# Performance work log

Measured on AMD Instinct MI355X. Metric: run time of the kernel, lower is better.

The kernel has to match this reference:

```python
import jax, jax.numpy as jnp
import numpy as np

B, S_LONG, S_SHORT, C_IN, H, D_STATE = 16384, 100, 10, 4, 64, 16
BN_EPS = 1e-5


def setup_inputs() -> dict:
    key = jax.random.key(0)
    ks = jax.random.split(key, 32)
    n = lambda i, shape, s=0.1: (jax.random.normal(ks[i], shape, dtype=jnp.float32) * s)
    inp = {
        "x": jax.random.normal(ks[0], (B, S_LONG, C_IN), dtype=jnp.float32),
        # ConvolutionalEyes (Conv1d weights are [out, in, k])
        "conv1_w": n(1, (H, C_IN, 3)), "conv1_b": n(2, (H,)),
        "conv2_w": n(3, (H, H, 5)),    "conv2_b": n(4, (H,)),
        "conv3_w": n(5, (H, H, 7)),    "conv3_b": n(6, (H,)),
        # BatchNorm1d (eval mode: running_mean=0, running_var=1)
        "bn1_g": jnp.ones((H,)), "bn1_b": jnp.zeros((H,)),
        "bn2_g": jnp.ones((H,)), "bn2_b": jnp.zeros((H,)),
        "bn3_g": jnp.ones((H,)), "bn3_b": jnp.zeros((H,)),
        # input_proj
        "proj_w": n(7, (C_IN, H)), "proj_b": n(8, (H,)),
        # MambaBlock (proj_in exists in torch code but is unused in forward)
        "A": n(9, (D_STATE, D_STATE)),
        "Bm": n(10, (H, D_STATE)),
        "Cm": n(11, (D_STATE, H)),
        "out_w": n(12, (H, H)), "out_b": n(13, (H,)),
        # ContextualGate
        "g1_w": n(14, (2 * H, H)), "g1_b": n(15, (H,)),
        "g2_w": n(16, (H, H)),     "g2_b": n(17, (H,)),
        # trading head
        "h1_w": n(18, (H, 32)), "h1_b": n(19, (32,)),
        "h2_w": n(20, (32, 3)), "h2_b": n(21, (3,)),
    }
    return inp


def _conv_bn_relu(x, w, b, g, beta, pad):
    # x: [B, C, L], w: [O, I, K]
    y = jax.lax.conv_general_dilated(x, w, (1,), [(pad, pad)],
                                     dimension_numbers=("NCW", "OIW", "NCW"))
    y = y + b[None, :, None]
    # eval-mode BN with running_mean=0, running_var=1
    y = g[None, :, None] * y * jax.lax.rsqrt(jnp.float32(1.0 + BN_EPS)) + beta[None, :, None]
    return jax.nn.relu(y)


def reference(x, conv1_w, conv1_b, conv2_w, conv2_b, conv3_w, conv3_b,
              bn1_g, bn1_b, bn2_g, bn2_b, bn3_g, bn3_b,
              proj_w, proj_b, A, Bm, Cm, out_w, out_b,
              g1_w, g1_b, g2_w, g2_b, h1_w, h1_b, h2_w, h2_b):
    # --- split windows ---
    x_short = x[:, -S_SHORT:, :]          # [B, 10, 4]
    x_long = x                            # [B, 100, 4]

    # --- ConvolutionalEyes (dropout = identity in eval) ---
    xc = jnp.swapaxes(x_short, 1, 2)      # [B, 4, 10]
    xc = _conv_bn_relu(xc, conv1_w, conv1_b, bn1_g, bn1_b, 1)
    xc = _conv_bn_relu(xc, conv2_w, conv2_b, bn2_g, bn2_b, 2)
    xc = _conv_bn_relu(xc, conv3_w, conv3_b, bn3_g, bn3_b, 3)
    short_features = jnp.mean(xc, axis=2)  # [B, 64]

    # --- input projection ---
    xp = x_long @ proj_w + proj_b          # [B, 100, 64]

    # --- MambaBlock: sequential scan over time ---
    def step(h, x_t):                      # h: [B, 16], x_t: [B, 64]
        h = jnp.tanh(x_t @ Bm + h @ A.T)
        return h, h @ Cm                   # y_t: [B, 64]

    h0 = jnp.zeros((x.shape[0], D_STATE), dtype=x.dtype)
    _, ys = jax.lax.scan(step, h0, jnp.swapaxes(xp, 0, 1))  # ys: [100, B, 64]
    long_context = ys[-1] @ out_w + out_b  # proj_out applied, last timestep

    # --- ContextualGate ---
    combined = jnp.concatenate([short_features, long_context], axis=1)  # [B, 128]
    gate = jax.nn.sigmoid(jnp.tanh(combined @ g1_w + g1_b) @ g2_w + g2_b)
    filtered = short_features * gate

    # --- trading head (dropout = identity in eval) ---
    logits = jax.nn.relu(filtered @ h1_w + h1_b) @ h2_w + h2_b  # [B, 3]
    return logits
```

## Files before the change

kernel.cpp:

```cpp
#include <hip/hip_runtime.h>
#include <cstddef>

#define NB 16384
#define TS 720
#define NRNN (NB/64)

typedef __attribute__((ext_vector_type(8))) _Float16 half8;
typedef __attribute__((ext_vector_type(4))) _Float16 half4;
typedef __attribute__((ext_vector_type(4))) float f32x4;
typedef __attribute__((ext_vector_type(2))) float f32x2;
typedef __attribute__((ext_vector_type(16))) float f32x16;

#define OFF_W1T 0
#define OFF_SC1 768
#define OFF_SH1 832
#define OFF_SC2 896
#define OFF_SH2 960
#define OFF_SC3 1024
#define OFF_SH3 1088
#define OFF_PB  1152
#define OFF_PBB 1216
#define OFF_W2H 2304
#define OFF_W2L 12544
#define OFF_W3H 22784
#define OFF_W3L 37120
#define OFF_SF  51456
#define OFF_H   (51456 + NB*64)
#define OFF_TF  1362176

#define G1H 0
#define G1L 8192
#define G2H 16384
#define G2L 20480
#define H1H 24576
#define H1L 26624
#define H2H 28672
#define H2L 29184
#define COH 29696
#define COL 30720
#define TFH 31744

static __device__ __forceinline__ f32x16 mfma32(half8 a, half8 b, f32x16 c) {
  return __builtin_amdgcn_mfma_f32_32x32x16_f16(a, b, c, 0, 0, 0);
}
static __device__ __forceinline__ f32x4 mfma16(half4 a, half4 b, f32x4 c) {
  return __builtin_amdgcn_mfma_f32_16x16x16f16(a, b, c, 0, 0, 0);
}
static __device__ __forceinline__ f32x4 mfma16k32(half8 a, half8 b, f32x4 c) {
  return __builtin_amdgcn_mfma_f32_16x16x32_f16(a, b, c, 0, 0, 0);
}

__global__ __launch_bounds__(256) void prep_kernel(
    const float* __restrict__ conv1_w, const float* __restrict__ conv1_b,
    const float* __restrict__ conv2_w, const float* __restrict__ conv2_b,
    const float* __restrict__ conv3_w, const float* __restrict__ conv3_b,
    const float* __restrict__ bn1_g, const float* __restrict__ bn1_b,
    const float* __restrict__ bn2_g, const float* __restrict__ bn2_b,
    const float* __restrict__ bn3_g, const float* __restrict__ bn3_b,
    const float* __restrict__ proj_w, const float* __restrict__ proj_b,
    const float* __restrict__ A, const float* __restrict__ Bm,
    const float* __restrict__ Cm, const float* __restrict__ out_w,
    const float* __restrict__ g1_w, const float* __restrict__ g2_w,
    const float* __restrict__ h1_w, const float* __restrict__ h2_w,
    float* __restrict__ ws)
{
  int tid = blockIdx.x * blockDim.x + threadIdx.x;
  int nt = gridDim.x * blockDim.x;
  const float s = rsqrtf(1.0f + 1e-5f);

  for (int i = tid; i < 64*12; i += nt) {
    int o = i & 63, rk = i >> 6;
    ws[OFF_W1T + i] = conv1_w[o*12 + rk];
  }
  for (int o = tid; o < 64; o += nt) {
    float s1 = bn1_g[o]*s, s2 = bn2_g[o]*s, s3 = bn3_g[o]*s;
    ws[OFF_SC1+o] = s1; ws[OFF_SH1+o] = s1*conv1_b[o] + bn1_b[o];
    ws[OFF_SC2+o] = s2; ws[OFF_SH2+o] = s2*conv2_b[o] + bn2_b[o];
    ws[OFF_SC3+o] = s3; ws[OFF_SH3+o] = s3*conv3_b[o] + bn3_b[o];
  }
  {
    _Float16* w2h = (_Float16*)(ws + OFF_W2H);
    _Float16* w2l = (_Float16*)(ws + OFF_W2L);
    for (int i = tid; i < 20*2*64; i += nt) {
      int lane = i & 63, ot = (i >> 6) & 1, sk = i >> 7;
      int tap = sk >> 2, ic0 = (sk & 3)*16 + (lane >> 5)*8;
      int o = ot*32 + (lane & 31);
      #pragma unroll
      for (int j = 0; j < 8; ++j) {
        float w = conv2_w[o*320 + (ic0 + j)*5 + tap];
        _Float16 hi = (_Float16)w;
        w2h[(size_t)i*8 + j] = hi;
        w2l[(size_t)i*8 + j] = (_Float16)(w - (float)hi);
      }
    }
  }
  {
    _Float16* w3h = (_Float16*)(ws + OFF_W3H);
    _Float16* w3l = (_Float16*)(ws + OFF_W3L);
    for (int i = tid; i < 28*2*64; i += nt) {
      int lane = i & 63, ot = (i >> 6) & 1, sk = i >> 7;
      int tap = sk >> 2, ic0 = (sk & 3)*16 + (lane >> 5)*8;
      int o = ot*32 + (lane & 31);
      #pragma unroll
      for (int j = 0; j < 8; ++j) {
        float w = conv3_w[o*448 + (ic0 + j)*7 + tap];
        _Float16 hi = (_Float16)w;
        w3h[(size_t)i*8 + j] = hi;
        w3l[(size_t)i*8 + j] = (_Float16)(w - (float)hi);
      }
    }
  }
  for (int i = tid; i < 64; i += nt) {
    int c = i >> 4, j = i & 15;
    float acc = 0.f;
    for (int m = 0; m < 64; ++m) acc += proj_w[c*64+m]*Bm[m*16+j];
    ws[OFF_PB + i] = acc;
  }
  for (int j = tid; j < 16; j += nt) {
    float acc = 0.f;
    for (int m = 0; m < 64; ++m) acc += proj_b[m]*Bm[m*16+j];
    ws[OFF_PBB + j] = acc;
  }

  _Float16* tf = (_Float16*)(ws + OFF_TF);
  for (int i = tid; i < 16*64; i += nt) {
    int l = i & 63, f = i >> 6, mt = f >> 2, ks = f & 3;
    int o = mt*16 + (l & 15), kb = ks*32 + (l >> 4)*8;
    #pragma unroll
    for (int j = 0; j < 8; ++j) {
      float w = g1_w[(size_t)(kb + j)*64 + o];
      _Float16 hi = (_Float16)w;
      tf[G1H + (size_t)i*8 + j] = hi;
      tf[G1L + (size_t)i*8 + j] = (_Float16)(w - (float)hi);
    }
  }
  for (int i = tid; i < 8*64; i += nt) {
    int l = i & 63, f = i >> 6, mt = f >> 1, ks = f & 1;
    int o = mt*16 + (l & 15), kb = ks*32 + (l >> 4)*8;
    #pragma unroll
    for (int j = 0; j < 8; ++j) {
      float w = g2_w[(size_t)(kb + j)*64 + o];
      _Float16 hi = (_Float16)w;
      tf[G2H + (size_t)i*8 + j] = hi;
      tf[G2L + (size_t)i*8 + j] = (_Float16)(w - (float)hi);
    }
  }
  for (int i = tid; i < 4*64; i += nt) {
    int l = i & 63, f = i >> 6, mt = f >> 1, ks = f & 1;
    int hx = mt*16 + (l & 15), kb = ks*32 + (l >> 4)*8;
    #pragma unroll
    for (int j = 0; j < 8; ++j) {
      float w = h1_w[(size_t)(kb + j)*32 + hx];
      _Float16 hi = (_Float16)w;
      tf[H1H + (size_t)i*8 + j] = hi;
      tf[H1L + (size_t)i*8 + j] = (_Float16)(w - (float)hi);
    }
  }
  for (int i = tid; i < 64; i += nt) {
    int l = i, m = l & 15, kb = (l >> 4)*8;
    #pragma unroll
    for (int j = 0; j < 8; ++j) {
      float w = (m < 3) ? h2_w[(size_t)(kb + j)*3 + m] : 0.f;
      _Float16 hi = (_Float16)w;
      tf[H2H + (size_t)i*8 + j] = hi;
      tf[H2L + (size_t)i*8 + j] = (_Float16)(w - (float)hi);
    }
  }
  for (int i = tid; i < 4*64; i += nt) {
    int l = i & 63, mt = i >> 6;
    int o = mt*16 + (l & 15), kb = (l >> 4)*4;
    #pragma unroll
    for (int j = 0; j < 4; ++j) {
      float acc = 0.f;
      for (int m = 0; m < 64; ++m) acc += Cm[(kb + j)*64 + m]*out_w[m*64 + o];
      _Float16 hi = (_Float16)acc;
      tf[COH + (size_t)i*4 + j] = hi;
      tf[COL + (size_t)i*4 + j] = (_Float16)(acc - (float)hi);
    }
  }
}

__global__ __launch_bounds__(256, 3) void conv123_kernel(
    const float* __restrict__ x, const float* __restrict__ wsr,
    const float* __restrict__ A, float* __restrict__ hout,
    float* __restrict__ sfp)
{
  __shared__ __align__(16) _Float16 ah[16][TS], al[16][TS];

  const int tid = threadIdx.x;
  const int lane = tid & 63;
  const int wid = tid >> 6;

  if (blockIdx.x < NRNN) {
    const int colb = lane & 15;
    const int q = lane >> 4;
    const size_t b = ((size_t)blockIdx.x*4 + wid)*16 + colb;

    const f32x4 av = *(const f32x4*)(A + (size_t)(lane & 15)*16 + q*4);
    half4 Ahi, Alo;
    #pragma unroll
    for (int j = 0; j < 4; ++j) {
      _Float16 hi = (_Float16)av[j];
      Ahi[j] = hi;
      Alo[j] = (_Float16)(av[j] - (float)hi);
    }
    f32x4 pb0 = *(const f32x4*)(wsr + OFF_PB + 0*16 + q*4);
    f32x4 pb1 = *(const f32x4*)(wsr + OFF_PB + 1*16 + q*4);
    f32x4 pb2 = *(const f32x4*)(wsr + OFF_PB + 2*16 + q*4);
    f32x4 pb3 = *(const f32x4*)(wsr + OFF_PB + 3*16 + q*4);
    f32x4 pbb = *(const f32x4*)(wsr + OFF_PBB + q*4);

    const float* xb = x + b*400;
    half4 hh = {}, hl = {};
    f32x4 hf;
    #pragma unroll 2
    for (int t = 0; t < 100; ++t) {
      const f32x4 xv = *(const f32x4*)(xb + t*4);
      f32x4 U;
      #pragma unroll
      for (int r = 0; r < 4; ++r)
        U[r] = pbb[r] + xv[0]*pb0[r] + xv[1]*pb1[r] + xv[2]*pb2[r] + xv[3]*pb3[r];
      f32x4 u = mfma16(Alo, hh, U);
      u = mfma16(Ahi, hl, u);
      u = mfma16(Ahi, hh, u);
      #pragma unroll
      for (int r = 0; r < 4; ++r) {
        float e = __expf(2.f*u[r]);
        float hn = 1.f - 2.f/(e + 1.f);
        hf[r] = hn;
        _Float16 hi = (_Float16)hn;
        hh[r] = hi;
        hl[r] = (_Float16)(hn - (float)hi);
      }
    }
    *(f32x4*)(hout + b*16 + q*4) = hf;
    return;
  }

  const int n = lane & 15;
  const int nc = (n < 10) ? n : 9;
  const int kh8 = (lane >> 5) * 8;
  const int rq = 4 * (lane >> 5);
  const int lbA = 4*wid + ((lane >> 4) & 1);
  const int lbB = lbA + 2;
  const half8 z8 = {};
  const size_t B0g = (size_t)(blockIdx.x - NRNN) * 16;

  {
    const float sc1 = wsr[OFF_SC1 + lane], sh1 = wsr[OFF_SH1 + lane];
    #pragma unroll
    for (int bb = 0; bb < 4; ++bb) {
      const int lb = 4*wid + bb;
      const size_t gb = B0g + lb;
      float xv[4][12];
      #pragma unroll
      for (int c = 0; c < 4; ++c) { xv[c][0] = 0.f; xv[c][11] = 0.f; }
      #pragma unroll
      for (int tt = 0; tt < 10; ++tt) {
        const f32x4 xt = *(const f32x4*)(x + gb*400 + (90 + tt)*4);
        #pragma unroll
        for (int c = 0; c < 4; ++c) xv[c][1 + tt] = xt[c];
      }
      float a1[10];
      #pragma unroll
      for (int t = 0; t < 10; ++t) a1[t] = 0.f;
      #pragma unroll
      for (int c = 0; c < 4; ++c)
        #pragma unroll
        for (int k = 0; k < 3; ++k) {
          const float wv = wsr[OFF_W1T + (c*3 + k)*64 + lane];
          #pragma unroll
          for (int t = 0; t < 10; ++t) a1[t] += wv * xv[c][t + k];
        }
      #pragma unroll
      for (int t = 0; t < 10; ++t) {
        float v = sc1*a1[t] + sh1;
        v = v > 0.f ? v : 0.f;
        _Float16 hi = (_Float16)v;
        ah[lb][t*72 + lane] = hi;
        al[lb][t*72 + lane] = (_Float16)(v - (float)hi);
      }
    }
  }

  const _Float16* bhpA = &ah[lbA][0];
  const _Float16* blpA = &al[lbA][0];
  const _Float16* bhpB = &ah[lbB][0];
  const _Float16* blpB = &al[lbB][0];
  const _Float16* w2h = (const _Float16*)(wsr + OFF_W2H);
  const _Float16* w2l = (const _Float16*)(wsr + OFF_W2L);
  const _Float16* w3h = (const _Float16*)(wsr + OFF_W3H);
  const _Float16* w3l = (const _Float16*)(wsr + OFF_W3L);
  const int lw8 = lane*8;

  {
    f32x16 a0A, a1A, a0B, a1B;
    #pragma unroll
    for (int r = 0; r < 16; ++r) { a0A[r] = 0.f; a1A[r] = 0.f; a0B[r] = 0.f; a1B[r] = 0.f; }
    #pragma unroll
    for (int sk = 0; sk < 20; ++sk) {
      const int tap = sk >> 2, icb = (sk & 3)*16;
      const int t = nc + tap - 2;
      const int tc = t < 0 ? 0 : (t > 9 ? 9 : t);
      const bool valid = (t >= 0) & (t <= 9);
      const int off = tc*72 + icb + kh8;
      half8 bhA = *(const half8*)(bhpA + off);
      half8 blA = *(const half8*)(blpA + off);
      half8 bhB = *(const half8*)(bhpB + off);
      half8 blB = *(const half8*)(blpB + off);
      bhA = valid ? bhA : z8;
      blA = valid ? blA : z8;
      bhB = valid ? bhB : z8;
      blB = valid ? blB : z8;
      const half8 wh0 = *(const half8*)(w2h + (size_t)(sk*2 + 0)*512 + lw8);
      const half8 wh1 = *(const half8*)(w2h + (size_t)(sk*2 + 1)*512 + lw8);
      const half8 wl0 = *(const half8*)(w2l + (size_t)(sk*2 + 0)*512 + lw8);
      const half8 wl1 = *(const half8*)(w2l + (size_t)(sk*2 + 1)*512 + lw8);
      a0A = mfma32(wh0, bhA, a0A);
      a0A = mfma32(wh0, blA, a0A);
      a0A = mfma32(wl0, bhA, a0A);
      a1A = mfma32(wh1, bhA, a1A);
      a1A = mfma32(wh1, blA, a1A);
      a1A = mfma32(wl1, bhA, a1A);
      a0B = mfma32(wh0, bhB, a0B);
      a0B = mfma32(wh0, blB, a0B);
      a0B = mfma32(wl0, bhB, a0B);
      a1B = mfma32(wh1, bhB, a1B);
      a1B = mfma32(wh1, blB, a1B);
      a1B = mfma32(wl1, bhB, a1B);
    }
    if (n < 10) {
      auto epi = [&](const f32x16& ac, int ot, int lb) {
        #pragma unroll
        for (int q = 0; q < 4; ++q) {
          const int rowb = 8*q + rq + ot*32;
          const f32x4 sc = *(const f32x4*)(wsr + OFF_SC2 + rowb);
          const f32x4 sh = *(const f32x4*)(wsr + OFF_SH2 + rowb);
          half4 h4, l4;
          #pragma unroll
          for (int r = 0; r < 4; ++r) {
            float v = sc[r]*ac[4*q + r] + sh[r];
            v = v > 0.f ? v : 0.f;
            _Float16 hi = (_Float16)v;
            h4[r] = hi;
            l4[r] = (_Float16)(v - (float)hi);
          }
          *(half4*)(&ah[lb][n*72 + rowb]) = h4;
          *(half4*)(&al[lb][n*72 + rowb]) = l4;
        }
      };
      epi(a0A, 0, lbA);
      epi(a1A, 1, lbA);
      epi(a0B, 0, lbB);
      epi(a1B, 1, lbB);
    }
  }

  {
    f32x16 b0A, b1A, b0B, b1B;
    #pragma unroll
    for (int r = 0; r < 16; ++r) { b0A[r] = 0.f; b1A[r] = 0.f; b0B[r] = 0.f; b1B[r] = 0.f; }
    #pragma unroll
    for (int sk = 0; sk < 28; ++sk) {
      const int tap = sk >> 2, icb = (sk & 3)*16;
      const int t = nc + tap - 3;
      const int tc = t < 0 ? 0 : (t > 9 ? 9 : t);
      const bool valid = (t >= 0) & (t <= 9);
      const int off = tc*72 + icb + kh8;
      half8 bhA = *(const half8*)(bhpA + off);
      half8 blA = *(const half8*)(blpA + off);
      half8 bhB = *(const half8*)(bhpB + off);
      half8 blB = *(const half8*)(blpB + off);
      bhA = valid ? bhA : z8;
      blA = valid ? blA : z8;
      bhB = valid ? bhB : z8;
      blB = valid ? blB : z8;
      const half8 wh0 = *(const half8*)(w3h + (size_t)(sk*2 + 0)*512 + lw8);
      const half8 wh1 = *(const half8*)(w3h + (size_t)(sk*2 + 1)*512 + lw8);
      const half8 wl0 = *(const half8*)(w3l + (size_t)(sk*2 + 0)*512 + lw8);
      const half8 wl1 = *(const half8*)(w3l + (size_t)(sk*2 + 1)*512 + lw8);
      b0A = mfma32(wh0, bhA, b0A);
      b0A = mfma32(wh0, blA, b0A);
      b0A = mfma32(wl0, bhA, b0A);
      b1A = mfma32(wh1, bhA, b1A);
      b1A = mfma32(wh1, blA, b1A);
      b1A = mfma32(wl1, bhA, b1A);
      b0B = mfma32(wh0, bhB, b0B);
      b0B = mfma32(wh0, blB, b0B);
      b0B = mfma32(wl0, bhB, b0B);
      b1B = mfma32(wh1, bhB, b1B);
      b1B = mfma32(wh1, blB, b1B);
      b1B = mfma32(wl1, bhB, b1B);
    }
    auto epi = [&](const f32x16& ac, int ot, int lb) {
      #pragma unroll
      for (int q = 0; q < 4; ++q) {
        const int rowb = 8*q + rq + ot*32;
        const f32x4 sc = *(const f32x4*)(wsr + OFF_SC3 + rowb);
        const f32x4 sh = *(const f32x4*)(wsr + OFF_SH3 + rowb);
        f32x4 v;
        #pragma unroll
        for (int r = 0; r < 4; ++r) {
          float t2 = sc[r]*ac[4*q + r] + sh[r];
          t2 = t2 > 0.f ? t2 : 0.f;
          v[r] = (n < 10) ? t2 : 0.f;
        }
        #pragma unroll
        for (int r = 0; r < 4; ++r) {
          v[r] += __shfl_xor(v[r], 1, 16);
          v[r] += __shfl_xor(v[r], 2, 16);
          v[r] += __shfl_xor(v[r], 4, 16);
          v[r] += __shfl_xor(v[r], 8, 16);
        }
        if (n == 0)
          *(f32x4*)(sfp + (B0g + lb)*64 + rowb) = v * 0.1f;
      }
    };
    epi(b0A, 0, lbA);
    epi(b1A, 1, lbA);
    epi(b0B, 0, lbB);
    epi(b1B, 1, lbB);
  }
}

#define CMBH 0
#define CMBL 2176
#define T1H  4352
#define T1L  5504
#define FLH  6656
#define FLL  7808
#define RH   8960
#define RL   9600
__global__ __launch_bounds__(256, 2) void tail_kernel(
    const float* __restrict__ wsr,
    const float* __restrict__ g1_b, const float* __restrict__ g2_b,
    const float* __restrict__ h1_b, const float* __restrict__ h2_b,
    const float* __restrict__ out_b, float* __restrict__ out)
{
  __shared__ __align__(16) _Float16 sAct[4*10240];

  const int tid = threadIdx.x;
  const int lane = tid & 63;
  const int wid = tid >> 6;
  const int n = lane & 15;
  const int q = lane >> 4;
  const int B0 = blockIdx.x*64 + wid*16;

  const _Float16* tfg = (const _Float16*)(wsr + OFF_TF);
  _Float16* wa = sAct + wid*10240;
  const float* sf = wsr + OFF_SF;
  const float* hws = wsr + OFF_H;

  const f32x4 hv = *(const f32x4*)(hws + (size_t)(B0 + n)*16 + q*4);
  half4 hh, hl;
  #pragma unroll
  for (int j = 0; j < 4; ++j) {
    _Float16 hi = (_Float16)hv[j];
    hh[j] = hi;
    hl[j] = (_Float16)(hv[j] - (float)hi);
  }
  f32x4 lc[4];
  #pragma unroll
  for (int mt = 0; mt < 4; ++mt) {
    lc[mt] = *(const f32x4*)(out_b + mt*16 + q*4);
    const half4 ah = *(const half4*)(tfg + COH + (size_t)(mt*64 + lane)*4);
    const half4 al = *(const half4*)(tfg + COL + (size_t)(mt*64 + lane)*4);
    lc[mt] = mfma16(al, hh, lc[mt]);
    lc[mt] = mfma16(ah, hl, lc[mt]);
    lc[mt] = mfma16(ah, hh, lc[mt]);
  }
  f32x4 sfv[4];
  #pragma unroll
  for (int mt = 0; mt < 4; ++mt) {
    sfv[mt] = *(const f32x4*)(sf + (size_t)(B0 + n)*64 + mt*16 + q*4);
    half4 sh4, sl4, lh4, ll4;
    #pragma unroll
    for (int r = 0; r < 4; ++r) {
      _Float16 hi = (_Float16)sfv[mt][r];
      sh4[r] = hi; sl4[r] = (_Float16)(sfv[mt][r] - (float)hi);
      _Float16 hi2 = (_Float16)lc[mt][r];
      lh4[r] = hi2; ll4[r] = (_Float16)(lc[mt][r] - (float)hi2);
    }
    *(half4*)(wa + CMBH + n*136 + mt*16 + q*4) = sh4;
    *(half4*)(wa + CMBL + n*136 + mt*16 + q*4) = sl4;
    *(half4*)(wa + CMBH + n*136 + 64 + mt*16 + q*4) = lh4;
    *(half4*)(wa + CMBL + n*136 + 64 + mt*16 + q*4) = ll4;
  }
  f32x4 u1[4];
  #pragma unroll
  for (int mt = 0; mt < 4; ++mt) u1[mt] = *(const f32x4*)(g1_b + mt*16 + q*4);
  #pragma unroll
  for (int ks = 0; ks < 4; ++ks) {
    const half8 bh = *(const half8*)(wa + CMBH + n*136 + ks*32 + q*8);
    const half8 bl = *(const half8*)(wa + CMBL + n*136 + ks*32 + q*8);
    #pragma unroll
    for (int mt = 0; mt < 4; ++mt) {
      const half8 ah = *(const half8*)(tfg + G1H + (size_t)((mt*4 + ks)*64 + lane)*8);
      const half8 al = *(const half8*)(tfg + G1L + (size_t)((mt*4 + ks)*64 + lane)*8);
      u1[mt] = mfma16k32(al, bh, u1[mt]);
      u1[mt] = mfma16k32(ah, bl, u1[mt]);
      u1[mt] = mfma16k32(ah, bh, u1[mt]);
    }
  }
  #pragma unroll
  for (int mt = 0; mt < 4; ++mt) {
    half4 th4, tl4;
    #pragma unroll
    for (int r = 0; r < 4; ++r) {
      float e = __expf(2.f*u1[mt][r]);
      float t1 = 1.f - 2.f/(e + 1.f);
      _Float16 hi = (_Float16)t1;
      th4[r] = hi; tl4[r] = (_Float16)(t1 - (float)hi);
    }
    *(half4*)(wa + T1H + n*72 + mt*16 + q*4) = th4;
    *(half4*)(wa + T1L + n*72 + mt*16 + q*4) = tl4;
  }
  f32x4 u2[4];
  #pragma unroll
  for (int mt = 0; mt < 4; ++mt) u2[mt] = *(const f32x4*)(g2_b + mt*16 + q*4);
  #pragma unroll
  for (int ks = 0; ks < 2; ++ks) {
    const half8 bh = *(const half8*)(wa + T1H + n*72 + ks*32 + q*8);
    const half8 bl = *(const half8*)(wa + T1L + n*72 + ks*32 + q*8);
    #pragma unroll
    for (int mt = 0; mt < 4; ++mt) {
      const half8 ah = *(const half8*)(tfg + G2H + (size_t)((mt*2 + ks)*64 + lane)*8);
      const half8 al = *(const half8*)(tfg + G2L + (size_t)((mt*2 + ks)*64 + lane)*8);
      u2[mt] = mfma16k32(al, bh, u2[mt]);
      u2[mt] = mfma16k32(ah, bl, u2[mt]);
      u2[mt] = mfma16k32(ah, bh, u2[mt]);
    }
  }
  #pragma unroll
  for (int mt = 0; mt < 4; ++mt) {
    half4 fh4, fl4;
    #pragma unroll
    for (int r = 0; r < 4; ++r) {
      float gate = 1.f/(1.f + __expf(-u2[mt][r]));
      float f = sfv[mt][r] * gate;
      _Float16 hi = (_Float16)f;
      fh4[r] = hi; fl4[r] = (_Float16)(f - (float)hi);
    }
    *(half4*)(wa + FLH + n*72 + mt*16 + q*4) = fh4;
    *(half4*)(wa + FLL + n*72 + mt*16 + q*4) = fl4;
  }
  f32x4 u3[2];
  #pragma unroll
  for (int mt = 0; mt < 2; ++mt) u3[mt] = *(const f32x4*)(h1_b + mt*16 + q*4);
  #pragma unroll
  for (int ks = 0; ks < 2; ++ks) {
    const half8 bh = *(const half8*)(wa + FLH + n*72 + ks*32 + q*8);
    const half8 bl = *(const half8*)(wa + FLL + n*72 + ks*32 + q*8);
    #pragma unroll
    for (int mt = 0; mt < 2; ++mt) {
      const half8 ah = *(const half8*)(tfg + H1H + (size_t)((mt*2 + ks)*64 + lane)*8);
      const half8 al = *(const half8*)(tfg + H1L + (size_t)((mt*2 + ks)*64 + lane)*8);
      u3[mt] = mfma16k32(al, bh, u3[mt]);
      u3[mt] = mfma16k32(ah, bl, u3[mt]);
      u3[mt] = mfma16k32(ah, bh, u3[mt]);
    }
  }
  #pragma unroll
  for (int mt = 0; mt < 2; ++mt) {
    half4 rh4, rl4;
    #pragma unroll
    for (int r = 0; r < 4; ++r) {
      float v = fmaxf(u3[mt][r], 0.f);
      _Float16 hi = (_Float16)v;
      rh4[r] = hi; rl4[r] = (_Float16)(v - (float)hi);
    }
    *(half4*)(wa + RH + n*40 + mt*16 + q*4) = rh4;
    *(half4*)(wa + RL + n*40 + mt*16 + q*4) = rl4;
  }
  {
    f32x4 u4;
    if (q == 0) { u4[0] = h2_b[0]; u4[1] = h2_b[1]; u4[2] = h2_b[2]; u4[3] = 0.f; }
    else { u4[0] = 0.f; u4[1] = 0.f; u4[2] = 0.f; u4[3] = 0.f; }
    const half8 bh = *(const half8*)(wa + RH + n*40 + q*8);
    const half8 bl = *(const half8*)(wa + RL + n*40 + q*8);
    const half8 ah = *(const half8*)(tfg + H2H + (size_t)lane*8);
    const half8 al = *(const half8*)(tfg + H2L + (size_t)lane*8);
    u4 = mfma16k32(al, bh, u4);
    u4 = mfma16k32(ah, bl, u4);
    u4 = mfma16k32(ah, bh, u4);
    if (q == 0) {
      out[(size_t)(B0 + n)*3 + 0] = u4[0];
      out[(size_t)(B0 + n)*3 + 1] = u4[1];
      out[(size_t)(B0 + n)*3 + 2] = u4[2];
    }
  }
}

extern "C" void kernel_launch(void* const* d_in, const int* in_sizes, int n_in,
                              void* d_out, int out_size, void* d_ws, size_t ws_size,
                              hipStream_t stream) {
  const float* x       = (const float*)d_in[0];
  const float* conv1_w = (const float*)d_in[1];
  const float* conv1_b = (const float*)d_in[2];
  const float* conv2_w = (const float*)d_in[3];
  const float* conv2_b = (const float*)d_in[4];
  const float* conv3_w = (const float*)d_in[5];
  const float* conv3_b = (const float*)d_in[6];
  const float* bn1_g   = (const float*)d_in[7];
  const float* bn1_b   = (const float*)d_in[8];
  const float* bn2_g   = (const float*)d_in[9];
  const float* bn2_b   = (const float*)d_in[10];
  const float* bn3_g   = (const float*)d_in[11];
  const float* bn3_b   = (const float*)d_in[12];
  const float* proj_w  = (const float*)d_in[13];
  const float* proj_b  = (const float*)d_in[14];
  const float* A       = (const float*)d_in[15];
  const float* Bm      = (const float*)d_in[16];
  const float* Cm      = (const float*)d_in[17];
  const float* out_w   = (const float*)d_in[18];
  const float* out_b   = (const float*)d_in[19];
  const float* g1_w    = (const float*)d_in[20];
  const float* g1_b    = (const float*)d_in[21];
  const float* g2_w    = (const float*)d_in[22];
  const float* g2_b    = (const float*)d_in[23];
  const float* h1_w    = (const float*)d_in[24];
  const float* h1_b    = (const float*)d_in[25];
  const float* h2_w    = (const float*)d_in[26];
  const float* h2_b    = (const float*)d_in[27];
  float* ws = (float*)d_ws;
  float* out = (float*)d_out;

  prep_kernel<<<64, 256, 0, stream>>>(conv1_w, conv1_b, conv2_w, conv2_b,
      conv3_w, conv3_b, bn1_g, bn1_b, bn2_g, bn2_b, bn3_g, bn3_b,
      proj_w, proj_b, A, Bm, Cm, out_w, g1_w, g2_w, h1_w, h2_w, ws);

  conv123_kernel<<<NRNN + NB/16, 256, 0, stream>>>(x, ws, A, ws + OFF_H,
      ws + OFF_SF);

  tail_kernel<<<NB/64, 256, 0, stream>>>(ws, g1_b, g2_b, h1_b, h2_b, out_b, out);
}
```

Baseline: 232.3 us.

## Fuse RNN scan and gate/head tail into conv kernel per 16-batch block

Removes the separate RNN blocks and the tail kernel. Each conv block now keeps its short features in shared memory, and after a barrier wave 0 runs the 100-step scan for its 16 batch rows and then the gate and head MLPs, reusing the conv LDS buffer. This drops a kernel launch and the global round trips for the hidden state and short features. The cost is that the long serial scan now runs on one wave after the conv phase instead of concurrently, so three waves sit idle and per-block latency grows.

```diff
diff --git a/kernel.cpp b/kernel.cpp
--- a/kernel.cpp
+++ b/kernel.cpp
@@ -3,7 +3,6 @@
 
 #define NB 16384
 #define TS 720
-#define NRNN (NB/64)
 
 typedef __attribute__((ext_vector_type(8))) _Float16 half8;
 typedef __attribute__((ext_vector_type(4))) _Float16 half4;
@@ -24,9 +23,7 @@
 #define OFF_W2L 12544
 #define OFF_W3H 22784
 #define OFF_W3L 37120
-#define OFF_SF  51456
-#define OFF_H   (51456 + NB*64)
-#define OFF_TF  1362176
+#define OFF_TF  51456
 
 #define G1H 0
 #define G1L 8192
@@ -39,6 +36,15 @@
 #define COH 29696
 #define COL 30720
 #define TFH 31744
+
+#define CMBH 0
+#define CMBL 2176
+#define T1H  4352
+#define T1L  5504
+#define FLH  6656
+#define FLL  7808
+#define RH   8960
+#define RL   9600
 
 static __device__ __forceinline__ f32x16 mfma32(half8 a, half8 b, f32x16 c) {
   return __builtin_amdgcn_mfma_f32_32x32x16_f16(a, b, c, 0, 0, 0);
@@ -182,60 +188,17 @@
 
 __global__ __launch_bounds__(256, 3) void conv123_kernel(
     const float* __restrict__ x, const float* __restrict__ wsr,
-    const float* __restrict__ A, float* __restrict__ hout,
-    float* __restrict__ sfp)
+    const float* __restrict__ A,
+    const float* __restrict__ g1_b, const float* __restrict__ g2_b,
+    const float* __restrict__ h1_b, const float* __restrict__ h2_b,
+    const float* __restrict__ out_b, float* __restrict__ out)
 {
   __shared__ __align__(16) _Float16 ah[16][TS], al[16][TS];
+  __shared__ __align__(16) float sfl[16][64];
 
   const int tid = threadIdx.x;
   const int lane = tid & 63;
   const int wid = tid >> 6;
-
-  if (blockIdx.x < NRNN) {
-    const int colb = lane & 15;
-    const int q = lane >> 4;
-    const size_t b = ((size_t)blockIdx.x*4 + wid)*16 + colb;
-
-    const f32x4 av = *(const f32x4*)(A + (size_t)(lane & 15)*16 + q*4);
-    half4 Ahi, Alo;
-    #pragma unroll
-    for (int j = 0; j < 4; ++j) {
-      _Float16 hi = (_Float16)av[j];
-      Ahi[j] = hi;
-      Alo[j] = (_Float16)(av[j] - (float)hi);
-    }
-    f32x4 pb0 = *(const f32x4*)(wsr + OFF_PB + 0*16 + q*4);
-    f32x4 pb1 = *(const f32x4*)(wsr + OFF_PB + 1*16 + q*4);
-    f32x4 pb2 = *(const f32x4*)(wsr + OFF_PB + 2*16 + q*4);
-    f32x4 pb3 = *(const f32x4*)(wsr + OFF_PB + 3*16 + q*4);
-    f32x4 pbb = *(const f32x4*)(wsr + OFF_PBB + q*4);
-
-    const float* xb = x + b*400;
-    half4 hh = {}, hl = {};
-    f32x4 hf;
-    #pragma unroll 2
-    for (int t = 0; t < 100; ++t) {
-      const f32x4 xv = *(const f32x4*)(xb + t*4);
-      f32x4 U;
-      #pragma unroll
-      for (int r = 0; r < 4; ++r)
-        U[r] = pbb[r] + xv[0]*pb0[r] + xv[1]*pb1[r] + xv[2]*pb2[r] + xv[3]*pb3[r];
-      f32x4 u = mfma16(Alo, hh, U);
-      u = mfma16(Ahi, hl, u);
-      u = mfma16(Ahi, hh, u);
-      #pragma unroll
-      for (int r = 0; r < 4; ++r) {
-        float e = __expf(2.f*u[r]);
-        float hn = 1.f - 2.f/(e + 1.f);
-        hf[r] = hn;
-        _Float16 hi = (_Float16)hn;
-        hh[r] = hi;
-        hl[r] = (_Float16)(hn - (float)hi);
-      }
-    }
-    *(f32x4*)(hout + b*16 + q*4) = hf;
-    return;
-  }
 
   const int n = lane & 15;
   const int nc = (n < 10) ? n : 9;
@@ -244,7 +207,7 @@
   const int lbA = 4*wid + ((lane >> 4) & 1);
   const int lbB = lbA + 2;
   const half8 z8 = {};
-  const size_t B0g = (size_t)(blockIdx.x - NRNN) * 16;
+  const size_t B0g = (size_t)blockIdx.x * 16;
 
   {
     const float sc1 = wsr[OFF_SC1 + lane], sh1 = wsr[OFF_SH1 + lane];
@@ -413,7 +376,7 @@
           v[r] += __shfl_xor(v[r], 8, 16);
         }
         if (n == 0)
-          *(f32x4*)(sfp + (B0g + lb)*64 + rowb) = v * 0.1f;
+          *(f32x4*)(&sfl[lb][rowb]) = v * 0.1f;
       }
     };
     epi(b0A, 0, lbA);
@@ -421,172 +384,193 @@
     epi(b0B, 0, lbB);
     epi(b1B, 1, lbB);
   }
-}
-
-#define CMBH 0
-#define CMBL 2176
-#define T1H  4352
-#define T1L  5504
-#define FLH  6656
-#define FLL  7808
-#define RH   8960
-#define RL   9600
-__global__ __launch_bounds__(256, 2) void tail_kernel(
-    const float* __restrict__ wsr,
-    const float* __restrict__ g1_b, const float* __restrict__ g2_b,
-    const float* __restrict__ h1_b, const float* __restrict__ h2_b,
-    const float* __restrict__ out_b, float* __restrict__ out)
-{
-  __shared__ __align__(16) _Float16 sAct[4*10240];
-
-  const int tid = threadIdx.x;
-  const int lane = tid & 63;
-  const int wid = tid >> 6;
-  const int n = lane & 15;
+
+  __syncthreads();
+  if (wid != 0) return;
+
+  const int colb = lane & 15;
   const int q = lane >> 4;
-  const int B0 = blockIdx.x*64 + wid*16;
-
-  const _Float16* tfg = (const _Float16*)(wsr + OFF_TF);
-  _Float16* wa = sAct + wid*10240;
-  const float* sf = wsr + OFF_SF;
-  const float* hws = wsr + OFF_H;
-
-  const f32x4 hv = *(const f32x4*)(hws + (size_t)(B0 + n)*16 + q*4);
-  half4 hh, hl;
-  #pragma unroll
-  for (int j = 0; j < 4; ++j) {
-    _Float16 hi = (_Float16)hv[j];
-    hh[j] = hi;
-    hl[j] = (_Float16)(hv[j] - (float)hi);
-  }
-  f32x4 lc[4];
-  #pragma unroll
-  for (int mt = 0; mt < 4; ++mt) {
-    lc[mt] = *(const f32x4*)(out_b + mt*16 + q*4);
-    const half4 ah = *(const half4*)(tfg + COH + (size_t)(mt*64 + lane)*4);
-    const half4 al = *(const half4*)(tfg + COL + (size_t)(mt*64 + lane)*4);
-    lc[mt] = mfma16(al, hh, lc[mt]);
-    lc[mt] = mfma16(ah, hl, lc[mt]);
-    lc[mt] = mfma16(ah, hh, lc[mt]);
-  }
-  f32x4 sfv[4];
-  #pragma unroll
-  for (int mt = 0; mt < 4; ++mt) {
-    sfv[mt] = *(const f32x4*)(sf + (size_t)(B0 + n)*64 + mt*16 + q*4);
-    half4 sh4, sl4, lh4, ll4;
-    #pragma unroll
-    for (int r = 0; r < 4; ++r) {
-      _Float16 hi = (_Float16)sfv[mt][r];
-      sh4[r] = hi; sl4[r] = (_Float16)(sfv[mt][r] - (float)hi);
-      _Float16 hi2 = (_Float16)lc[mt][r];
-      lh4[r] = hi2; ll4[r] = (_Float16)(lc[mt][r] - (float)hi2);
-    }
-    *(half4*)(wa + CMBH + n*136 + mt*16 + q*4) = sh4;
-    *(half4*)(wa + CMBL + n*136 + mt*16 + q*4) = sl4;
-    *(half4*)(wa + CMBH + n*136 + 64 + mt*16 + q*4) = lh4;
-    *(half4*)(wa + CMBL + n*136 + 64 + mt*16 + q*4) = ll4;
-  }
-  f32x4 u1[4];
-  #pragma unroll
-  for (int mt = 0; mt < 4; ++mt) u1[mt] = *(const f32x4*)(g1_b + mt*16 + q*4);
-  #pragma unroll
-  for (int ks = 0; ks < 4; ++ks) {
-    const half8 bh = *(const half8*)(wa + CMBH + n*136 + ks*32 + q*8);
-    const half8 bl = *(const half8*)(wa + CMBL + n*136 + ks*32 + q*8);
+  f32x4 hf;
+  {
+    const size_t b = B0g + colb;
+    const f32x4 av = *(const f32x4*)(A + (size_t)colb*16 + q*4);
+    half4 Ahi, Alo;
+    #pragma unroll
+    for (int j = 0; j < 4; ++j) {
+      _Float16 hi = (_Float16)av[j];
+      Ahi[j] = hi;
+      Alo[j] = (_Float16)(av[j] - (float)hi);
+    }
+    f32x4 pb0 = *(const f32x4*)(wsr + OFF_PB + 0*16 + q*4);
+    f32x4 pb1 = *(const f32x4*)(wsr + OFF_PB + 1*16 + q*4);
+    f32x4 pb2 = *(const f32x4*)(wsr + OFF_PB + 2*16 + q*4);
+    f32x4 pb3 = *(const f32x4*)(wsr + OFF_PB + 3*16 + q*4);
+    f32x4 pbb = *(const f32x4*)(wsr + OFF_PBB + q*4);
+
+    const float* xb = x + b*400;
+    half4 hh = {}, hl = {};
+    #pragma unroll 2
+    for (int t = 0; t < 100; ++t) {
+      const f32x4 xv = *(const f32x4*)(xb + t*4);
+      f32x4 U;
+      #pragma unroll
+      for (int r = 0; r < 4; ++r)
+        U[r] = pbb[r] + xv[0]*pb0[r] + xv[1]*pb1[r] + xv[2]*pb2[r] + xv[3]*pb3[r];
+      f32x4 u = mfma16(Alo, hh, U);
+      u = mfma16(Ahi, hl, u);
+      u = mfma16(Ahi, hh, u);
+      #pragma unroll
+      for (int r = 0; r < 4; ++r) {
+        float e = __expf(2.f*u[r]);
+        float hn = 1.f - 2.f/(e + 1.f);
+        hf[r] = hn;
+        _Float16 hi = (_Float16)hn;
+        hh[r] = hi;
+        hl[r] = (_Float16)(hn - (float)hi);
+      }
+    }
+  }
+
+  {
+    const _Float16* tfg = (const _Float16*)(wsr + OFF_TF);
+    _Float16* wa = &ah[0][0];
+
+    half4 hh, hl;
+    #pragma unroll
+    for (int j = 0; j < 4; ++j) {
+      _Float16 hi = (_Float16)hf[j];
+      hh[j] = hi;
+      hl[j] = (_Float16)(hf[j] - (float)hi);
+    }
+    f32x4 lc[4];
     #pragma unroll
     for (int mt = 0; mt < 4; ++mt) {
-      const half8 ah = *(const half8*)(tfg + G1H + (size_t)((mt*4 + ks)*64 + lane)*8);
-      const half8 al = *(const half8*)(tfg + G1L + (size_t)((mt*4 + ks)*64 + lane)*8);
-      u1[mt] = mfma16k32(al, bh, u1[mt]);
-      u1[mt] = mfma16k32(ah, bl, u1[mt]);
-      u1[mt] = mfma16k32(ah, bh, u1[mt]);
-    }
-  }
-  #pragma unroll
-  for (int mt = 0; mt < 4; ++mt) {
-    half4 th4, tl4;
-    #pragma unroll
-    for (int r = 0; r < 4; ++r) {
-      float e = __expf(2.f*u1[mt][r]);
-      float t1 = 1.f - 2.f/(e + 1.f);
-      _Float16 hi = (_Float16)t1;
-      th4[r] = hi; tl4[r] = (_Float16)(t1 - (float)hi);
-    }
-    *(half4*)(wa + T1H + n*72 + mt*16 + q*4) = th4;
-    *(half4*)(wa + T1L + n*72 + mt*16 + q*4) = tl4;
-  }
-  f32x4 u2[4];
-  #pragma unroll
-  for (int mt = 0; mt < 4; ++mt) u2[mt] = *(const f32x4*)(g2_b + mt*16 + q*4);
-  #pragma unroll
-  for (int ks = 0; ks < 2; ++ks) {
-    const half8 bh = *(const half8*)(wa + T1H + n*72 + ks*32 + q*8);
-    const half8 bl = *(const half8*)(wa + T1L + n*72 + ks*32 + q*8);
+      lc[mt] = *(const f32x4*)(out_b + mt*16 + q*4);
+      const half4 ca = *(const half4*)(tfg + COH + (size_t)(mt*64 + lane)*4);
+      const half4 cl = *(const half4*)(tfg + COL + (size_t)(mt*64 + lane)*4);
+      lc[mt] = mfma16(cl, hh, lc[mt]);
+      lc[mt] = mfma16(ca, hl, lc[mt]);
+      lc[mt] = mfma16(ca, hh, lc[mt]);
+    }
+    f32x4 sfv[4];
     #pragma unroll
     for (int mt = 0; mt < 4; ++mt) {
-      const half8 ah = *(const half8*)(tfg + G2H + (size_t)((mt*2 + ks)*64 + lane)*8);
-      const half8 al = *(const half8*)(tfg + G2L + (size_t)((mt*2 + ks)*64 + lane)*8);
-      u2[mt] = mfma16k32(al, bh, u2[mt]);
-      u2[mt] = mfma16k32(ah, bl, u2[mt]);
-      u2[mt] = mfma16k32(ah, bh, u2[mt]);
-    }
-  }
-  #pragma unroll
-  for (int mt = 0; mt < 4; ++mt) {
-    half4 fh4, fl4;
-    #pragma unroll
-    for (int r = 0; r < 4; ++r) {
-      float gate = 1.f/(1.f + __expf(-u2[mt][r]));
-      float f = sfv[mt][r] * gate;
-      _Float16 hi = (_Float16)f;
-      fh4[r] = hi; fl4[r] = (_Float16)(f - (float)hi);
-    }
-    *(half4*)(wa + FLH + n*72 + mt*16 + q*4) = fh4;
-    *(half4*)(wa + FLL + n*72 + mt*16 + q*4) = fl4;
-  }
-  f32x4 u3[2];
-  #pragma unroll
-  for (int mt = 0; mt < 2; ++mt) u3[mt] = *(const f32x4*)(h1_b + mt*16 + q*4);
-  #pragma unroll
-  for (int ks = 0; ks < 2; ++ks) {
-    const half8 bh = *(const half8*)(wa + FLH + n*72 + ks*32 + q*8);
-    const half8 bl = *(const half8*)(wa + FLL + n*72 + ks*32 + q*8);
+      sfv[mt] = *(const f32x4*)(&sfl[n][mt*16 + q*4]);
+      half4 sh4, sl4, lh4, ll4;
+      #pragma unroll
+      for (int r = 0; r < 4; ++r) {
+        _Float16 hi = (_Float16)sfv[mt][r];
+        sh4[r] = hi; sl4[r] = (_Float16)(sfv[mt][r] - (float)hi);
+        _Float16 hi2 = (_Float16)lc[mt][r];
+        lh4[r] = hi2; ll4[r] = (_Float16)(lc[mt][r] - (float)hi2);
+      }
+      *(half4*)(wa + CMBH + n*136 + mt*16 + q*4) = sh4;
+      *(half4*)(wa + CMBL + n*136 + mt*16 + q*4) = sl4;
+      *(half4*)(wa + CMBH + n*136 + 64 + mt*16 + q*4) = lh4;
+      *(half4*)(wa + CMBL + n*136 + 64 + mt*16 + q*4) = ll4;
+    }
+    f32x4 u1[4];
+    #pragma unroll
+    for (int mt = 0; mt < 4; ++mt) u1[mt] = *(const f32x4*)(g1_b + mt*16 + q*4);
+    #pragma unroll
+    for (int ks = 0; ks < 4; ++ks) {
+      const half8 bh = *(const half8*)(wa + CMBH + n*136 + ks*32 + q*8);
+      const half8 bl = *(const half8*)(wa + CMBL + n*136 + ks*32 + q*8);
+      #pragma unroll
+      for (int mt = 0; mt < 4; ++mt) {
+        const half8 fa = *(const half8*)(tfg + G1H + (size_t)((mt*4 + ks)*64 + lane)*8);
+        const half8 fl = *(const half8*)(tfg + G1L + (size_t)((mt*4 + ks)*64 + lane)*8);
+        u1[mt] = mfma16k32(fl, bh, u1[mt]);
+        u1[mt] = mfma16k32(fa, bl, u1[mt]);
+        u1[mt] = mfma16k32(fa, bh, u1[mt]);
+      }
+    }
+    #pragma unroll
+    for (int mt = 0; mt < 4; ++mt) {
+      half4 th4, tl4;
+      #pragma unroll
+      for (int r = 0; r < 4; ++r) {
+        float e = __expf(2.f*u1[mt][r]);
+        float t1 = 1.f - 2.f/(e + 1.f);
+        _Float16 hi = (_Float16)t1;
+        th4[r] = hi; tl4[r] = (_Float16)(t1 - (float)hi);
+      }
+      *(half4*)(wa + T1H + n*72 + mt*16 + q*4) = th4;
+      *(half4*)(wa + T1L + n*72 + mt*16 + q*4) = tl4;
+    }
+    f32x4 u2[4];
+    #pragma unroll
+    for (int mt = 0; mt < 4; ++mt) u2[mt] = *(const f32x4*)(g2_b + mt*16 + q*4);
+    #pragma unroll
+    for (int ks = 0; ks < 2; ++ks) {
+      const half8 bh = *(const half8*)(wa + T1H + n*72 + ks*32 + q*8);
+      const half8 bl = *(const half8*)(wa + T1L + n*72 + ks*32 + q*8);
+      #pragma unroll
+      for (int mt = 0; mt < 4; ++mt) {
+        const half8 fa = *(const half8*)(tfg + G2H + (size_t)((mt*2 + ks)*64 + lane)*8);
+        const half8 fl = *(const half8*)(tfg + G2L + (size_t)((mt*2 + ks)*64 + lane)*8);
+        u2[mt] = mfma16k32(fl, bh, u2[mt]);
+        u2[mt] = mfma16k32(fa, bl, u2[mt]);
+        u2[mt] = mfma16k32(fa, bh, u2[mt]);
+      }
+    }
+    #pragma unroll
+    for (int mt = 0; mt < 4; ++mt) {
+      half4 fh4, fl4;
+      #pragma unroll
+      for (int r = 0; r < 4; ++r) {
+        float gate = 1.f/(1.f + __expf(-u2[mt][r]));
+        float f = sfv[mt][r] * gate;
+        _Float16 hi = (_Float16)f;
+        fh4[r] = hi; fl4[r] = (_Float16)(f - (float)hi);
+      }
+      *(half4*)(wa + FLH + n*72 + mt*16 + q*4) = fh4;
+      *(half4*)(wa + FLL + n*72 + mt*16 + q*4) = fl4;
+    }
+    f32x4 u3[2];
+    #pragma unroll
+    for (int mt = 0; mt < 2; ++mt) u3[mt] = *(const f32x4*)(h1_b + mt*16 + q*4);
+    #pragma unroll
+    for (int ks = 0; ks < 2; ++ks) {
+      const half8 bh = *(const half8*)(wa + FLH + n*72 + ks*32 + q*8);
+      const half8 bl = *(const half8*)(wa + FLL + n*72 + ks*32 + q*8);
+      #pragma unroll
+      for (int mt = 0; mt < 2; ++mt) {
+        const half8 fa = *(const half8*)(tfg + H1H + (size_t)((mt*2 + ks)*64 + lane)*8);
+        const half8 fl = *(const half8*)(tfg + H1L + (size_t)((mt*2 + ks)*64 + lane)*8);
+        u3[mt] = mfma16k32(fl, bh, u3[mt]);
+        u3[mt] = mfma16k32(fa, bl, u3[mt]);
+        u3[mt] = mfma16k32(fa, bh, u3[mt]);
+      }
+    }
     #pragma unroll
     for (int mt = 0; mt < 2; ++mt) {
-      const half8 ah = *(const half8*)(tfg + H1H + (size_t)((mt*2 + ks)*64 + lane)*8);
-      const half8 al = *(const half8*)(tfg + H1L + (size_t)((mt*2 + ks)*64 + lane)*8);
-      u3[mt] = mfma16k32(al, bh, u3[mt]);
-      u3[mt] = mfma16k32(ah, bl, u3[mt]);
-      u3[mt] = mfma16k32(ah, bh, u3[mt]);
-    }
-  }
-  #pragma unroll
-  for (int mt = 0; mt < 2; ++mt) {
-    half4 rh4, rl4;
-    #pragma unroll
-    for (int r = 0; r < 4; ++r) {
-      float v = fmaxf(u3[mt][r], 0.f);
-      _Float16 hi = (_Float16)v;
-      rh4[r] = hi; rl4[r] = (_Float16)(v - (float)hi);
-    }
-    *(half4*)(wa + RH + n*40 + mt*16 + q*4) = rh4;
-    *(half4*)(wa + RL + n*40 + mt*16 + q*4) = rl4;
-  }
-  {
-    f32x4 u4;
-    if (q == 0) { u4[0] = h2_b[0]; u4[1] = h2_b[1]; u4[2] = h2_b[2]; u4[3] = 0.f; }
-    else { u4[0] = 0.f; u4[1] = 0.f; u4[2] = 0.f; u4[3] = 0.f; }
-    const half8 bh = *(const half8*)(wa + RH + n*40 + q*8);
-    const half8 bl = *(const half8*)(wa + RL + n*40 + q*8);
-    const half8 ah = *(const half8*)(tfg + H2H + (size_t)lane*8);
-    const half8 al = *(const half8*)(tfg + H2L + (size_t)lane*8);
-    u4 = mfma16k32(al, bh, u4);
-    u4 = mfma16k32(ah, bl, u4);
-    u4 = mfma16k32(ah, bh, u4);
-    if (q == 0) {
-      out[(size_t)(B0 + n)*3 + 0] = u4[0];
-      out[(size_t)(B0 + n)*3 + 1] = u4[1];
-      out[(size_t)(B0 + n)*3 + 2] = u4[2];
+      half4 rh4, rl4;
+      #pragma unroll
+      for (int r = 0; r < 4; ++r) {
+        float v = fmaxf(u3[mt][r], 0.f);
+        _Float16 hi = (_Float16)v;
+        rh4[r] = hi; rl4[r] = (_Float16)(v - (float)hi);
+      }
+      *(half4*)(wa + RH + n*40 + mt*16 + q*4) = rh4;
+      *(half4*)(wa + RL + n*40 + mt*16 + q*4) = rl4;
+    }
+    {
+      f32x4 u4;
+      if (q == 0) { u4[0] = h2_b[0]; u4[1] = h2_b[1]; u4[2] = h2_b[2]; u4[3] = 0.f; }
+      else { u4[0] = 0.f; u4[1] = 0.f; u4[2] = 0.f; u4[3] = 0.f; }
+      const half8 bh = *(const half8*)(wa + RH + n*40 + q*8);
+      const half8 bl = *(const half8*)(wa + RL + n*40 + q*8);
+      const half8 fa = *(const half8*)(tfg + H2H + (size_t)lane*8);
+      const half8 fl = *(const half8*)(tfg + H2L + (size_t)lane*8);
+      u4 = mfma16k32(fl, bh, u4);
+      u4 = mfma16k32(fa, bl, u4);
+      u4 = mfma16k32(fa, bh, u4);
+      if (q == 0) {
+        out[(size_t)(B0g + n)*3 + 0] = u4[0];
+        out[(size_t)(B0g + n)*3 + 1] = u4[1];
+        out[(size_t)(B0g + n)*3 + 2] = u4[2];
+      }
     }
   }
 }
@@ -629,8 +613,6 @@
       conv3_w, conv3_b, bn1_g, bn1_b, bn2_g, bn2_b, bn3_g, bn3_b,
       proj_w, proj_b, A, Bm, Cm, out_w, g1_w, g2_w, h1_w, h2_w, ws);
 
-  conv123_kernel<<<NRNN + NB/16, 256, 0, stream>>>(x, ws, A, ws + OFF_H,
-      ws + OFF_SF);
-
-  tail_kernel<<<NB/64, 256, 0, stream>>>(ws, g1_b, g2_b, h1_b, h2_b, out_b, out);
+  conv123_kernel<<<NB/16, 256, 0, stream>>>(x, ws, A,
+      g1_b, g2_b, h1_b, h2_b, out_b, out);
 }
```

New measurement: 289.9 us. 1.25x slower.
